# Kernel tuning notes

Measured on AMD Instinct MI355X. Metric: run time of the kernel, lower is better.

Reference implementation:

```python
import jax, jax.numpy as jnp
import numpy as np

N_NODES = 50000
N_EDGES = 800000
C_IN = 128
C_OUT = 128
K = 6


def setup_inputs() -> dict:
    key = jax.random.key(0)
    ks = jax.random.split(key, 8)
    nodes = jax.random.normal(ks[0], (N_NODES, C_IN), dtype=jnp.float32)
    edges = jax.random.uniform(ks[1], (N_EDGES,), dtype=jnp.float32)
    senders = jax.random.randint(ks[2], (N_EDGES,), 0, N_NODES, dtype=jnp.int32)
    receivers = jax.random.randint(ks[3], (N_EDGES,), 0, N_NODES, dtype=jnp.int32)
    # K independent Dense(out_channels) layers (kernel + bias each), plus extra module bias
    W = jax.random.normal(ks[4], (K, C_IN, C_OUT), dtype=jnp.float32) / jnp.sqrt(jnp.float32(C_IN))
    b_dense = jax.random.normal(ks[5], (K, C_OUT), dtype=jnp.float32) * 0.01
    bias = jnp.zeros((C_OUT,), dtype=jnp.float32)
    return {"nodes": nodes, "edges": edges, "senders": senders, "receivers": receivers,
            "W": W, "b_dense": b_dense, "bias": bias}


def reference(nodes, edges, senders, receivers, W, b_dense, bias):
    n = nodes.shape[0]
    # Laplacian L = D - A with A[s, r] = w. deg_i = sum of weights of edges with sender i.
    deg = jax.ops.segment_sum(edges, senders, num_segments=n)
    # lambda_max = 2 * max(L.data) where L.data = concat(deg, -edges)
    lambda_max = 2.0 * jnp.maximum(deg.max(), (-edges).max())
    scale = 2.0 / lambda_max  # L_hat = (2/lambda_max) * L

    def Lmatvec(x):  # (2L/lambda_max) @ x via gather + segment_sum
        agg = jax.ops.segment_sum(edges[:, None] * x[receivers], senders, num_segments=n)
        return scale * (deg[:, None] * x - agg)

    Tx0 = nodes
    out = Tx0 @ W[0] + b_dense[0]
    Tx1 = Lmatvec(Tx0)
    out = out + Tx1 @ W[1] + b_dense[1]
    for k in range(2, K):
        Tx2 = 2.0 * Lmatvec(Tx1) - Tx0
        out = out + Tx2 @ W[k] + b_dense[k]
        Tx0, Tx1 = Tx1, Tx2
    return out + bias
```

## Files before the change

### kernel.cpp

```cpp
#include <hip/hip_runtime.h>

#define C 128
#define KORD 6
#define KD (KORD * C)
#define EPB 4096

typedef __attribute__((ext_vector_type(8))) short short8;
typedef __attribute__((ext_vector_type(4))) float f32x4;

__device__ __forceinline__ short f2bf(float f) {
  unsigned u = __float_as_uint(f);
  unsigned r = (u + 0x7fffu + ((u >> 16) & 1u)) >> 16;
  return (short)r;
}
__device__ __forceinline__ float bf2f(short s) {
  return __uint_as_float(((unsigned)(unsigned short)s) << 16);
}

__device__ __forceinline__ unsigned enc_f32(float f) {
  unsigned u = __float_as_uint(f);
  return (u & 0x80000000u) ? ~u : (u | 0x80000000u);
}
__device__ __forceinline__ float dec_f32(unsigned u) {
  return (u & 0x80000000u) ? __uint_as_float(u ^ 0x80000000u) : __uint_as_float(~u);
}

__global__ void prep_kernel(const float* __restrict__ W, const float* __restrict__ bd,
                            const float* __restrict__ bias, short* __restrict__ Wt,
                            float* __restrict__ bsum, const float* __restrict__ nodes,
                            short* __restrict__ xb, int n) {
  int i = blockIdx.x * blockDim.x + threadIdx.x;
  if (i < KD * C) {
    int k = i >> 7, nn = i & 127;
    Wt[(size_t)nn * KD + k] = f2bf(W[i]);
  }
  if (i < C) {
    float s = bias[i];
#pragma unroll
    for (int k = 0; k < KORD; ++k) s += bd[k * C + i];
    bsum[i] = s;
  }
  if (i < n * 32) {
    int row = i >> 5, c4 = i & 31;
    float4 v = ((const float4*)nodes)[(size_t)row * 32 + c4];
    short4 o;
    o.x = f2bf(v.x); o.y = f2bf(v.y); o.z = f2bf(v.z); o.w = f2bf(v.w);
    ((short4*)(xb + (size_t)row * KD))[c4] = o;
  }
}

__global__ __launch_bounds__(256) void p1_count_kernel(const int* __restrict__ senders,
                                                       const float* __restrict__ edges, int ne,
                                                       int* __restrict__ hist, int NB,
                                                       unsigned* __restrict__ umax) {
  __shared__ int h[256];
  int t = threadIdx.x;
  h[t] = 0;
  __syncthreads();
  int base = blockIdx.x * EPB;
  int end = min(base + EPB, ne);
  float m = -INFINITY;
  for (int i = base + t; i < end; i += 256) {
    atomicAdd(&h[senders[i] >> 8], 1);
    m = fmaxf(m, -edges[i]);
  }
#pragma unroll
  for (int off = 32; off > 0; off >>= 1) m = fmaxf(m, __shfl_down(m, off, 64));
  if ((t & 63) == 0) atomicMax(umax, enc_f32(m));
  __syncthreads();
  hist[t * NB + blockIdx.x] = h[t];
}

__global__ __launch_bounds__(1024) void scan1_kernel(const int* __restrict__ counts,
                                                     int* __restrict__ offsets,
                                                     int* __restrict__ bsums, int n) {
  int t = threadIdx.x;
  int i = blockIdx.x * 1024 + t;
  int lane = t & 63, w = t >> 6;
  int v = (i < n) ? counts[i] : 0;
  int s = v;
#pragma unroll
  for (int d = 1; d < 64; d <<= 1) {
    int o = __shfl_up(s, d, 64);
    if (lane >= d) s += o;
  }
  __shared__ int wsum[16];
  if (lane == 63) wsum[w] = s;
  __syncthreads();
  if (t < 16) {
    int ws = wsum[t];
#pragma unroll
    for (int d = 1; d < 16; d <<= 1) {
      int o = __shfl_up(ws, d, 64);
      if (t >= d) ws += o;
    }
    wsum[t] = ws;
  }
  __syncthreads();
  int excl = s - v + (w > 0 ? wsum[w - 1] : 0);
  if (i < n) offsets[i] = excl;
  if (t == 1023) bsums[blockIdx.x] = wsum[15];
}

__global__ __launch_bounds__(1024) void scan2_kernel(int* __restrict__ bsums, int nb) {
  int t = threadIdx.x;
  int lane = t & 63, w = t >> 6;
  int v = (t < nb) ? bsums[t] : 0;
  int s = v;
#pragma unroll
  for (int d = 1; d < 64; d <<= 1) {
    int o = __shfl_up(s, d, 64);
    if (lane >= d) s += o;
  }
  __shared__ int wsum[16];
  if (lane == 63) wsum[w] = s;
  __syncthreads();
  if (t < 16) {
    int ws = wsum[t];
#pragma unroll
    for (int d = 1; d < 16; d <<= 1) {
      int o = __shfl_up(ws, d, 64);
      if (t >= d) ws += o;
    }
    wsum[t] = ws;
  }
  __syncthreads();
  int excl = s - v + (w > 0 ? wsum[w - 1] : 0);
  if (t < nb) bsums[t] = excl;
}

__global__ __launch_bounds__(256) void p1_scatter_kernel(
    const int* __restrict__ senders, const int* __restrict__ receivers,
    const float* __restrict__ edges, int ne, const int* __restrict__ scanned,
    const int* __restrict__ bsums, int NB, int2* __restrict__ bkt) {
  __shared__ int basec[256];
  int t = threadIdx.x;
  int idx = t * NB + blockIdx.x;
  basec[t] = scanned[idx] + bsums[idx >> 10];
  __syncthreads();
  int base = blockIdx.x * EPB;
  int end = min(base + EPB, ne);
  for (int i = base + t; i < end; i += 256) {
    int s = senders[i];
    int pos = atomicAdd(&basec[s >> 8], 1);
    int2 rec;
    rec.x = __float_as_int(edges[i]);
    rec.y = receivers[i] | ((s & 255) << 16);
    bkt[pos] = rec;
  }
}

__global__ __launch_bounds__(256) void p2_finalize_kernel(
    const int2* __restrict__ bkt, const int* __restrict__ scanned,
    const int* __restrict__ bsums, int NB, int NBUCK, int ne, int n, int2* __restrict__ csr_wr,
    int* __restrict__ offsets, float* __restrict__ degf, unsigned* __restrict__ umax,
    int* __restrict__ ticket, float* __restrict__ scalep) {
  __shared__ int h[256];
  __shared__ int cur[256];
  __shared__ float dg[256];
  __shared__ int wsum[4];
  __shared__ float wmax[4];
  int t = threadIdx.x;
  int b = blockIdx.x;
  int i0 = b * NB;
  int base = scanned[i0] + bsums[i0 >> 10];
  int bend = ne;
  if (b != NBUCK - 1) {
    int i1 = (b + 1) * NB;
    bend = scanned[i1] + bsums[i1 >> 10];
  }
  h[t] = 0;
  dg[t] = 0.f;
  __syncthreads();
  for (int i = base + t; i < bend; i += 256) atomicAdd(&h[(bkt[i].y >> 16) & 255], 1);
  __syncthreads();
  int lane = t & 63, w = t >> 6;
  int v = h[t];
  int s = v;
#pragma unroll
  for (int d = 1; d < 64; d <<= 1) {
    int o = __shfl_up(s, d, 64);
    if (lane >= d) s += o;
  }
  if (lane == 63) wsum[w] = s;
  __syncthreads();
  int carry = 0;
#pragma unroll
  for (int j = 0; j < 4; ++j) carry += (j < w) ? wsum[j] : 0;
  int excl = s - v + carry;
  int node = b * 256 + t;
  if (node < n) offsets[node] = base + excl;
  cur[t] = base + excl;
  __syncthreads();
  for (int i = base + t; i < bend; i += 256) {
    int2 rec = bkt[i];
    int bin = (rec.y >> 16) & 255;
    int pos = atomicAdd(&cur[bin], 1);
    int2 outrec;
    outrec.x = rec.x;
    outrec.y = rec.y & 0xFFFF;
    csr_wr[pos] = outrec;
    atomicAdd(&dg[bin], __int_as_float(rec.x));
  }
  __syncthreads();
  float d = dg[t];
  if (node < n) degf[node] = d;
  float m = (node < n) ? d : 0.f;
#pragma unroll
  for (int off = 32; off > 0; off >>= 1) m = fmaxf(m, __shfl_down(m, off, 64));
  if (lane == 0) wmax[w] = m;
  __syncthreads();
  if (t == 0) {
    float mm = fmaxf(fmaxf(wmax[0], wmax[1]), fmaxf(wmax[2], wmax[3]));
    atomicMax(umax, enc_f32(mm));
    if (b == NBUCK - 1) offsets[n] = ne;
    __threadfence();
    int done = atomicAdd(ticket, 1);
    if (done == NBUCK - 1) {
      unsigned cu = atomicMax(umax, 0u);
      scalep[0] = 1.0f / dec_f32(cu);
    }
  }
}

__global__ __launch_bounds__(256, 8) void matvec_kernel(
    const short* __restrict__ xg,
    const short* __restrict__ zg,
    short* __restrict__ yg,
    const float* __restrict__ deg, const int* __restrict__ offsets,
    const int2* __restrict__ csr_wr, const float* __restrict__ scalep, float coef, int n) {
  int wid = (blockIdx.x * blockDim.x + threadIdx.x) >> 6;
  int lane = threadIdx.x & 63;
  int sub = lane & 15;
  int quarter = lane >> 4;
  if (wid >= n) return;
  float sc = scalep[0] * coef;
  int e0 = offsets[wid], e1 = offsets[wid + 1];
  float d = 0.f;
  short8 xo, zv;
  if (quarter == 0) {
    d = deg[wid];
    xo = *(const short8*)(xg + (size_t)wid * KD + sub * 8);
    if (zg) zv = *(const short8*)(zg + (size_t)wid * KD + sub * 8);
  }
  float a[8];
#pragma unroll
  for (int j = 0; j < 8; ++j) a[j] = 0.f;
  int elast = e1 - 1;
  for (int e = e0 + quarter; e < e1; e += 16) {
    int eb1 = e + 4, eb2 = e + 8, eb3 = e + 12;
    int2 p0 = csr_wr[e];
    int2 p1 = csr_wr[min(eb1, elast)];
    int2 p2 = csr_wr[min(eb2, elast)];
    int2 p3 = csr_wr[min(eb3, elast)];
    short8 v0 = *(const short8*)(xg + (size_t)p0.y * KD + sub * 8);
    short8 v1 = *(const short8*)(xg + (size_t)p1.y * KD + sub * 8);
    short8 v2 = *(const short8*)(xg + (size_t)p2.y * KD + sub * 8);
    short8 v3 = *(const short8*)(xg + (size_t)p3.y * KD + sub * 8);
    float w0 = __int_as_float(p0.x);
    float w1 = (eb1 < e1) ? __int_as_float(p1.x) : 0.f;
    float w2 = (eb2 < e1) ? __int_as_float(p2.x) : 0.f;
    float w3 = (eb3 < e1) ? __int_as_float(p3.x) : 0.f;
#pragma unroll
    for (int j = 0; j < 8; ++j) {
      float t0 = fmaf(w0, bf2f(v0[j]), a[j]);
      float t1 = fmaf(w1, bf2f(v1[j]), t0);
      float t2 = fmaf(w2, bf2f(v2[j]), t1);
      a[j] = fmaf(w3, bf2f(v3[j]), t2);
    }
  }
#pragma unroll
  for (int j = 0; j < 8; ++j) {
    a[j] += __shfl_xor(a[j], 16, 64);
    a[j] += __shfl_xor(a[j], 32, 64);
  }
  if (quarter == 0) {
    float r[8];
#pragma unroll
    for (int j = 0; j < 8; ++j) r[j] = sc * fmaf(d, bf2f(xo[j]), -a[j]);
    if (zg) {
#pragma unroll
      for (int j = 0; j < 8; ++j) r[j] -= bf2f(zv[j]);
    }
    short8 o;
#pragma unroll
    for (int j = 0; j < 8; ++j) o[j] = f2bf(r[j]);
    *(short8*)(yg + (size_t)wid * KD + sub * 8) = o;
  }
}

#define BK 64
#define LDP (BK + 8)
__global__ __launch_bounds__(256) void mfma_gemm_kernel(const short* __restrict__ Xb,
                                                        const short* __restrict__ Wt,
                                                        const float* __restrict__ bsum,
                                                        float* __restrict__ out, int n) {
  __shared__ short Al[64 * LDP];
  __shared__ short Bl[128 * LDP];
  int t = threadIdx.x;
  int w = t >> 6, lane = t & 63;
  int m = lane & 15, q = lane >> 4;
  int row0 = blockIdx.x * 64;
  int c0 = w * 32;

  f32x4 acc[4][2];
#pragma unroll
  for (int i = 0; i < 4; ++i)
#pragma unroll
    for (int j = 0; j < 2; ++j) acc[i][j] = (f32x4){0.f, 0.f, 0.f, 0.f};

  for (int k0 = 0; k0 < KD; k0 += BK) {
    __syncthreads();
#pragma unroll
    for (int p = 0; p < 2; ++p) {
      int idx = t + 256 * p;
      int r = idx >> 3, u = idx & 7;
      int gr = min(row0 + r, n - 1);
      short8 v = *(const short8*)(Xb + (size_t)gr * KD + k0 + u * 8);
      *(short8*)(Al + r * LDP + u * 8) = v;
    }
#pragma unroll
    for (int p = 0; p < 4; ++p) {
      int idx = t + 256 * p;
      int cc = idx >> 3, u = idx & 7;
      short8 v = *(const short8*)(Wt + (size_t)cc * KD + k0 + u * 8);
      *(short8*)(Bl + cc * LDP + u * 8) = v;
    }
    __syncthreads();
#pragma unroll
    for (int s = 0; s < 2; ++s) {
      int ko = s * 32 + q * 8;
      short8 b0 = *(const short8*)(Bl + (c0 + m) * LDP + ko);
      short8 b1 = *(const short8*)(Bl + (c0 + 16 + m) * LDP + ko);
#pragma unroll
      for (int rt = 0; rt < 4; ++rt) {
        short8 av = *(const short8*)(Al + (rt * 16 + m) * LDP + ko);
        acc[rt][0] = __builtin_amdgcn_mfma_f32_16x16x32_bf16(av, b0, acc[rt][0], 0, 0, 0);
        acc[rt][1] = __builtin_amdgcn_mfma_f32_16x16x32_bf16(av, b1, acc[rt][1], 0, 0, 0);
      }
    }
  }

#pragma unroll
  for (int ct = 0; ct < 2; ++ct) {
    int col = c0 + ct * 16 + m;
    float bs = bsum[col];
#pragma unroll
    for (int rt = 0; rt < 4; ++rt) {
#pragma unroll
      for (int i = 0; i < 4; ++i) {
        int row = row0 + rt * 16 + q * 4 + i;
        if (row < n) out[(size_t)row * C + col] = acc[rt][ct][i] + bs;
      }
    }
  }
}

extern "C" void kernel_launch(void* const* d_in, const int* in_sizes, int n_in,
                              void* d_out, int out_size, void* d_ws, size_t ws_size,
                              hipStream_t stream) {
  const float* nodes = (const float*)d_in[0];
  const float* edges = (const float*)d_in[1];
  const int* senders = (const int*)d_in[2];
  const int* receivers = (const int*)d_in[3];
  const float* W = (const float*)d_in[4];
  const float* b_dense = (const float*)d_in[5];
  const float* bias = (const float*)d_in[6];
  float* out = (float*)d_out;
  int n = in_sizes[0] / C;
  int ne = in_sizes[1];
  int NB = (ne + EPB - 1) / EPB;
  int NBUCK = (n + 255) >> 8;
  int M = 256 * NB;
  int nb2 = (M + 1023) / 1024;

  char* ws = (char*)d_ws;
  size_t off = 0;
  auto alloc = [&](size_t b) { size_t r = off; off += (b + 255) & ~(size_t)255; return r; };
  float* degf = (float*)(ws + alloc((size_t)n * 4));
  int* offsets = (int*)(ws + alloc((size_t)(n + 1) * 4));
  int* hist = (int*)(ws + alloc((size_t)M * 4));
  int* bsums = (int*)(ws + alloc((size_t)nb2 * 4));
  int2* bkt = (int2*)(ws + alloc((size_t)ne * 8));
  int2* csr_wr = (int2*)(ws + alloc((size_t)ne * 8));
  unsigned* umax = (unsigned*)(ws + alloc(8));
  float* scalep = (float*)(ws + alloc(4));
  float* bsum = (float*)(ws + alloc(C * 4));
  short* Xb = (short*)(ws + alloc((size_t)n * KD * 2));
  short* Wt = (short*)(ws + alloc((size_t)KD * C * 2));
  (void)ws_size; (void)n_in; (void)out_size;

  hipMemsetAsync(umax, 0, 8, stream);

  int prep_n = max(KD * C, n * 32);
  prep_kernel<<<(prep_n + 255) / 256, 256, 0, stream>>>(W, b_dense, bias, Wt, bsum, nodes, Xb, n);

  p1_count_kernel<<<NB, 256, 0, stream>>>(senders, edges, ne, hist, NB, umax);
  scan1_kernel<<<nb2, 1024, 0, stream>>>(hist, hist, bsums, M);
  scan2_kernel<<<1, 1024, 0, stream>>>(bsums, nb2);
  p1_scatter_kernel<<<NB, 256, 0, stream>>>(senders, receivers, edges, ne, hist, bsums, NB, bkt);
  p2_finalize_kernel<<<NBUCK, 256, 0, stream>>>(bkt, hist, bsums, NB, NBUCK, ne, n, csr_wr,
                                                offsets, degf, umax, (int*)(umax + 1), scalep);

  int mvblocks = (n * 64 + 255) / 256;

  matvec_kernel<<<mvblocks, 256, 0, stream>>>(Xb + 0 * C, nullptr, Xb + 1 * C,
                                              degf, offsets, csr_wr, scalep, 1.0f, n);
  matvec_kernel<<<mvblocks, 256, 0, stream>>>(Xb + 1 * C, Xb + 0 * C, Xb + 2 * C,
                                              degf, offsets, csr_wr, scalep, 2.0f, n);
  matvec_kernel<<<mvblocks, 256, 0, stream>>>(Xb + 2 * C, Xb + 1 * C, Xb + 3 * C,
                                              degf, offsets, csr_wr, scalep, 2.0f, n);
  matvec_kernel<<<mvblocks, 256, 0, stream>>>(Xb + 3 * C, Xb + 2 * C, Xb + 4 * C,
                                              degf, offsets, csr_wr, scalep, 2.0f, n);
  matvec_kernel<<<mvblocks, 256, 0, stream>>>(Xb + 4 * C, Xb + 3 * C, Xb + 5 * C,
                                              degf, offsets, csr_wr, scalep, 2.0f, n);

  mfma_gemm_kernel<<<(n + 63) / 64, 256, 0, stream>>>(Xb, Wt, bsum, out, n);
}
```

Baseline: 327.7 us.

## Map two nodes per wavefront in matvec and precompute row offsets in CSR

```diff
diff --git a/kernel.cpp b/kernel.cpp
--- a/kernel.cpp
+++ b/kernel.cpp
@@ -3,7 +3,7 @@
 #define C 128
 #define KORD 6
 #define KD (KORD * C)
-#define EPB 4096
+#define EPB 2048
 
 typedef __attribute__((ext_vector_type(8))) short short8;
 typedef __attribute__((ext_vector_type(4))) float f32x4;
@@ -198,7 +198,7 @@
     int pos = atomicAdd(&cur[bin], 1);
     int2 outrec;
     outrec.x = rec.x;
-    outrec.y = rec.y & 0xFFFF;
+    outrec.y = (rec.y & 0xFFFF) * KD;
     csr_wr[pos] = outrec;
     atomicAdd(&dg[bin], __int_as_float(rec.x));
   }
@@ -231,36 +231,39 @@
     const int2* __restrict__ csr_wr, const float* __restrict__ scalep, float coef, int n) {
   int wid = (blockIdx.x * blockDim.x + threadIdx.x) >> 6;
   int lane = threadIdx.x & 63;
+  int hw = lane >> 5;
+  int qq = (lane >> 4) & 1;
   int sub = lane & 15;
-  int quarter = lane >> 4;
-  if (wid >= n) return;
+  if (2 * wid >= n) return;
+  int node = 2 * wid + hw;
+  int nd = min(node, n - 1);
   float sc = scalep[0] * coef;
-  int e0 = offsets[wid], e1 = offsets[wid + 1];
+  int e0 = offsets[nd], e1 = offsets[nd + 1];
   float d = 0.f;
   short8 xo, zv;
-  if (quarter == 0) {
-    d = deg[wid];
-    xo = *(const short8*)(xg + (size_t)wid * KD + sub * 8);
-    if (zg) zv = *(const short8*)(zg + (size_t)wid * KD + sub * 8);
+  if (qq == 0) {
+    d = deg[nd];
+    xo = *(const short8*)(xg + (size_t)nd * KD + sub * 8);
+    if (zg) zv = *(const short8*)(zg + (size_t)nd * KD + sub * 8);
   }
   float a[8];
 #pragma unroll
   for (int j = 0; j < 8; ++j) a[j] = 0.f;
   int elast = e1 - 1;
-  for (int e = e0 + quarter; e < e1; e += 16) {
-    int eb1 = e + 4, eb2 = e + 8, eb3 = e + 12;
+  const short* xs = xg + sub * 8;
+  for (int e = e0 + qq * 4; e < e1; e += 8) {
     int2 p0 = csr_wr[e];
-    int2 p1 = csr_wr[min(eb1, elast)];
-    int2 p2 = csr_wr[min(eb2, elast)];
-    int2 p3 = csr_wr[min(eb3, elast)];
-    short8 v0 = *(const short8*)(xg + (size_t)p0.y * KD + sub * 8);
-    short8 v1 = *(const short8*)(xg + (size_t)p1.y * KD + sub * 8);
-    short8 v2 = *(const short8*)(xg + (size_t)p2.y * KD + sub * 8);
-    short8 v3 = *(const short8*)(xg + (size_t)p3.y * KD + sub * 8);
+    int2 p1 = csr_wr[min(e + 1, elast)];
+    int2 p2 = csr_wr[min(e + 2, elast)];
+    int2 p3 = csr_wr[min(e + 3, elast)];
+    short8 v0 = *(const short8*)(xs + p0.y);
+    short8 v1 = *(const short8*)(xs + p1.y);
+    short8 v2 = *(const short8*)(xs + p2.y);
+    short8 v3 = *(const short8*)(xs + p3.y);
     float w0 = __int_as_float(p0.x);
-    float w1 = (eb1 < e1) ? __int_as_float(p1.x) : 0.f;
-    float w2 = (eb2 < e1) ? __int_as_float(p2.x) : 0.f;
-    float w3 = (eb3 < e1) ? __int_as_float(p3.x) : 0.f;
+    float w1 = (e + 1 < e1) ? __int_as_float(p1.x) : 0.f;
+    float w2 = (e + 2 < e1) ? __int_as_float(p2.x) : 0.f;
+    float w3 = (e + 3 < e1) ? __int_as_float(p3.x) : 0.f;
 #pragma unroll
     for (int j = 0; j < 8; ++j) {
       float t0 = fmaf(w0, bf2f(v0[j]), a[j]);
@@ -270,11 +273,8 @@
     }
   }
 #pragma unroll
-  for (int j = 0; j < 8; ++j) {
-    a[j] += __shfl_xor(a[j], 16, 64);
-    a[j] += __shfl_xor(a[j], 32, 64);
-  }
-  if (quarter == 0) {
+  for (int j = 0; j < 8; ++j) a[j] += __shfl_xor(a[j], 16, 64);
+  if (qq == 0 && node < n) {
     float r[8];
 #pragma unroll
     for (int j = 0; j < 8; ++j) r[j] = sc * fmaf(d, bf2f(xo[j]), -a[j]);
@@ -285,7 +285,7 @@
     short8 o;
 #pragma unroll
     for (int j = 0; j < 8; ++j) o[j] = f2bf(r[j]);
-    *(short8*)(yg + (size_t)wid * KD + sub * 8) = o;
+    *(short8*)(yg + (size_t)nd * KD + sub * 8) = o;
   }
 }
 
@@ -402,7 +402,7 @@
   p2_finalize_kernel<<<NBUCK, 256, 0, stream>>>(bkt, hist, bsums, NB, NBUCK, ne, n, csr_wr,
                                                 offsets, degf, umax, (int*)(umax + 1), scalep);
 
-  int mvblocks = (n * 64 + 255) / 256;
+  int mvblocks = (n * 32 + 255) / 256;
 
   matvec_kernel<<<mvblocks, 256, 0, stream>>>(Xb + 0 * C, nullptr, Xb + 1 * C,
                                               degf, offsets, csr_wr, scalep, 1.0f, n);
```

Measured after the change: 344.4 us. 5.1% more time.
